# Kernel tuning notes

Measured on AMD Instinct MI355X. Metric: run time of the kernel, lower is better.

The kernel has to match this reference:

```python
import jax, jax.numpy as jnp
import numpy as np

N, E = 50000, 800000
IN, HID, HEADS, OUT = 128, 32, 8, 40
D1 = HID * HEADS  # 256


def setup_inputs() -> dict:
    key = jax.random.key(0)
    ks = jax.random.split(key, 24)

    def w(k, fin, fout):
        return (jax.random.normal(k, (fin, fout), jnp.float32) / np.sqrt(fin)).astype(jnp.float32)

    def b(k, fout):
        return (jax.random.normal(k, (fout,), jnp.float32) * 0.02).astype(jnp.float32)

    inp = {
        "x": jax.random.normal(ks[0], (N, IN), jnp.float32),
        "edge_index": jax.random.randint(ks[1], (2, E), 0, N, dtype=jnp.int64),
        # layer 1: TransformerConv(IN -> HID, heads=HEADS, concat=True, beta=True)
        "q1w": w(ks[2], IN, D1), "q1b": b(ks[3], D1),
        "k1w": w(ks[4], IN, D1), "k1b": b(ks[5], D1),
        "v1w": w(ks[6], IN, D1), "v1b": b(ks[7], D1),
        "s1w": w(ks[8], IN, D1), "s1b": b(ks[9], D1),
        "b1w": w(ks[10], 3 * D1, 1),
        # layer 2: TransformerConv(D1 -> OUT, heads=1, concat=False, beta=True)
        "q2w": w(ks[11], D1, OUT), "q2b": b(ks[12], OUT),
        "k2w": w(ks[13], D1, OUT), "k2b": b(ks[14], OUT),
        "v2w": w(ks[15], D1, OUT), "v2b": b(ks[16], OUT),
        "s2w": w(ks[17], D1, OUT), "s2b": b(ks[18], OUT),
        "b2w": w(ks[19], 3 * OUT, 1),
    }
    return inp


def _tconv(x, src, dst, qw, qb, kw, kb, vw, vb, sw, sb, bw, heads, ch, concat):
    """PyG TransformerConv (no edge_attr, root_weight=True, beta=True), eval mode."""
    n = x.shape[0]
    q = (x @ qw + qb).reshape(n, heads, ch)
    k = (x @ kw + kb).reshape(n, heads, ch)
    v = (x @ vw + vb).reshape(n, heads, ch)
    # per-edge attention logits: message flows src(j) -> dst(i)
    alpha = jnp.einsum("ehc,ehc->eh", q[dst], k[src]) / np.sqrt(ch)  # [E,H]
    # segment softmax over incoming edges of each dst node
    amax = jax.ops.segment_max(alpha, dst, num_segments=n)  # [N,H]
    a = jnp.exp(alpha - amax[dst])
    asum = jax.ops.segment_sum(a, dst, num_segments=n)  # [N,H]
    attn = a / asum[dst]  # [E,H]
    # scatter-aggregate weighted values
    out = jax.ops.segment_sum(v[src] * attn[:, :, None], dst, num_segments=n)  # [N,H,C]
    out = out.reshape(n, heads * ch) if concat else out.mean(axis=1)
    skip = x @ sw + sb
    beta = jax.nn.sigmoid(jnp.concatenate([out, skip, out - skip], axis=-1) @ bw)  # [N,1]
    return beta * skip + (1.0 - beta) * out


def reference(x, edge_index, q1w, q1b, k1w, k1b, v1w, v1b, s1w, s1b, b1w,
              q2w, q2b, k2w, k2b, v2w, v2b, s2w, s2b, b2w):
    src, dst = edge_index[0], edge_index[1]
    h = jax.nn.elu(_tconv(x, src, dst, q1w, q1b, k1w, k1b, v1w, v1b, s1w, s1b, b1w, HEADS, HID, True))
    return _tconv(h, src, dst, q2w, q2b, k2w, k2b, v2w, v2b, s2w, s2b, b2w, 1, OUT, False)
```

## Files before the change

### kernel.cpp

```cpp
#include <hip/hip_runtime.h>
#include <cstdint>
#include <cstddef>

#define N_NODES 50000
#define N_EDGES 800000
#define IN_F    128
#define HID     32
#define HEADS   8
#define OUT_F   40
#define D1      256
#define W1COLS  1024
#define W2COLS  160
#define CAP     64

#define GFILL_B   3125
#define G1_BX     391
#define G1_BY     8
#define G1_GEMM_B (G1_BX * G1_BY)
#define G1_TOTAL  (GFILL_B + G1_GEMM_B)

typedef unsigned short ushortT;
typedef unsigned char  ucharT;
typedef unsigned long long ullT;
typedef unsigned short ushortx8 __attribute__((ext_vector_type(8)));
typedef __bf16 bf16x8 __attribute__((ext_vector_type(8)));
typedef float floatx4 __attribute__((ext_vector_type(4)));
typedef float floatx2 __attribute__((ext_vector_type(2)));

__device__ inline ushortT f2bf(float f) {
    union { float f; unsigned int u; } c; c.f = f;
    unsigned int r = c.u + 0x7FFFu + ((c.u >> 16) & 1u);
    return (ushortT)(r >> 16);
}
__device__ inline float bf2f(ushortT h) {
    union { unsigned int u; float f; } c; c.u = ((unsigned int)h) << 16; return c.f;
}

__device__ inline float red8(float x) {
    int v;
    v = __builtin_amdgcn_update_dpp(0, __float_as_int(x), 0xB1, 0xF, 0xF, false);
    x += __int_as_float(v);
    v = __builtin_amdgcn_update_dpp(0, __float_as_int(x), 0x4E, 0xF, 0xF, false);
    x += __int_as_float(v);
    v = __builtin_amdgcn_update_dpp(0, __float_as_int(x), 0x141, 0xF, 0xF, false);
    x += __int_as_float(v);
    return x;
}

#define PREP_CONV_B  6250
#define PREP_W1_B    512
#define PREP_W2_B    160
#define PREP_TOTAL_B (PREP_CONV_B + PREP_W1_B + PREP_W2_B)

__global__ __launch_bounds__(256) void k_prep(
        const float* __restrict__ x, ushortT* __restrict__ xb,
        const float* __restrict__ q1w, const float* __restrict__ k1w,
        const float* __restrict__ v1w, const float* __restrict__ s1w,
        const float* __restrict__ q1b, const float* __restrict__ k1b,
        const float* __restrict__ v1b, const float* __restrict__ s1b,
        ushortT* __restrict__ W1T, float* __restrict__ b1c,
        const float* __restrict__ q2w, const float* __restrict__ k2w,
        const float* __restrict__ v2w, const float* __restrict__ s2w,
        const float* __restrict__ q2b, const float* __restrict__ k2b,
        const float* __restrict__ v2b, const float* __restrict__ s2b,
        ushortT* __restrict__ W2T, float* __restrict__ b2c) {
    int b = blockIdx.x;
    int tid = threadIdx.x;
    if (b < PREP_CONV_B) {
        int i = b * 256 + tid;
        float4 v = reinterpret_cast<const float4*>(x)[i];
        ushort4 o;
        o.x = f2bf(v.x); o.y = f2bf(v.y); o.z = f2bf(v.z); o.w = f2bf(v.w);
        reinterpret_cast<ushort4*>(xb)[i] = o;
    } else if (b < PREP_CONV_B + PREP_W1_B) {
        int t = (b - PREP_CONV_B) * 256 + tid;
        int c = t / IN_F, k = t % IN_F;
        int sel = c >> 8, cc = c & 255;
        const float* w = sel == 0 ? q1w : sel == 1 ? k1w : sel == 2 ? v1w : s1w;
        W1T[(size_t)c * IN_F + k] = f2bf(w[(size_t)k * D1 + cc]);
        if (k == 0) {
            const float* bb = sel == 0 ? q1b : sel == 1 ? k1b : sel == 2 ? v1b : s1b;
            b1c[c] = bb[cc];
        }
    } else {
        int t = (b - PREP_CONV_B - PREP_W1_B) * 256 + tid;
        int c = t / D1, k = t % D1;
        int sel = c / OUT_F, cc = c % OUT_F;
        const float* w = sel == 0 ? q2w : sel == 1 ? k2w : sel == 2 ? v2w : s2w;
        W2T[(size_t)c * D1 + k] = f2bf(w[(size_t)k * OUT_F + cc]);
        if (k == 0) {
            const float* bb = sel == 0 ? q2b : sel == 1 ? k2b : sel == 2 ? v2b : s2b;
            b2c[c] = bb[cc];
        }
    }
}

template<int MODE>
__global__ __launch_bounds__(256) void gemm_mfma_pack(
        const ushortT* __restrict__ A, const ushortT* __restrict__ BT,
        const float* __restrict__ bias, float* __restrict__ QSf,
        ushortT* __restrict__ QSh, ucharT* __restrict__ KV8,
        ushortT* __restrict__ K2V2,
        const int* __restrict__ ei, int* __restrict__ cursor, int* __restrict__ col,
        int M, int K, int Nn) {
    constexpr int TM = 128, TN = 128, TK = 32, LDP = 40;
    __shared__ ushortT smem[TM * LDP + TN * LDP];
    ushortT* As = smem;
    ushortT* Bs = smem + TM * LDP;
    int bx2, by2;
    if (MODE == 1) {
        int t = blockIdx.x;
        int idx;
        bool isFill;
        if (t < 2 * GFILL_B) { isFill = !(t & 1); idx = t >> 1; }
        else                 { isFill = false;    idx = t - GFILL_B; }
        if (isFill) {
            int e = idx * 256 + threadIdx.x;
            if (e < N_EDGES) {
                int dd = ei[N_EDGES + e];
                int p = atomicAdd(&cursor[dd], 1);
                col[dd * CAP + p] = ei[e];
            }
            return;
        }
        bx2 = idx % G1_BX;
        by2 = idx / G1_BX;
    } else {
        bx2 = blockIdx.x;
        by2 = blockIdx.y;
    }
    int tid = threadIdx.x;
    int lane = tid & 63, wave = tid >> 6;
    int bm = bx2 * TM, bn = by2 * TN;
    int wm = (wave & 1) * 64, wn = (wave >> 1) * 64;
    int mrow = lane & 15, g = lane >> 4;
    floatx4 acc[4][4] = {};

    for (int k0 = 0; k0 < K; k0 += TK) {
#pragma unroll
        for (int it = 0; it < 2; ++it) {
            int idx = tid + it * 256;
            int r = idx >> 2, c = (idx & 3) * 8;
            int gm = bm + r;
            ushortx8 val;
            if (gm < M) val = *reinterpret_cast<const ushortx8*>(A + (size_t)gm * K + k0 + c);
            else        val = (ushortx8)0;
            *reinterpret_cast<ushortx8*>(As + r * LDP + c) = val;
        }
#pragma unroll
        for (int it = 0; it < 2; ++it) {
            int idx = tid + it * 256;
            int r = idx >> 2, c = (idx & 3) * 8;
            int gn = bn + r;
            ushortx8 val;
            if (gn < Nn) val = *reinterpret_cast<const ushortx8*>(BT + (size_t)gn * K + k0 + c);
            else         val = (ushortx8)0;
            *reinterpret_cast<ushortx8*>(Bs + r * LDP + c) = val;
        }
        __syncthreads();
        {
            bf16x8 a[4], b[4];
#pragma unroll
            for (int i = 0; i < 4; ++i)
                a[i] = *reinterpret_cast<const bf16x8*>(As + (wm + i * 16 + mrow) * LDP + g * 8);
#pragma unroll
            for (int j = 0; j < 4; ++j)
                b[j] = *reinterpret_cast<const bf16x8*>(Bs + (wn + j * 16 + mrow) * LDP + g * 8);
#pragma unroll
            for (int i = 0; i < 4; ++i)
#pragma unroll
                for (int j = 0; j < 4; ++j)
                    acc[i][j] = __builtin_amdgcn_mfma_f32_16x16x32_bf16(a[i], b[j], acc[i][j], 0, 0, 0);
        }
        __syncthreads();
    }

    if (MODE == 1) {
        float* lds = reinterpret_cast<float*>(smem) + wave * 1088;
        int sec = by2 >> 1;
        int ccbase = (by2 & 1) * 128 + wn;
        int cb4 = (lane & 15) * 4;
        int rlo = lane >> 4;
        float4 bv = *reinterpret_cast<const float4*>(bias + by2 * 128 + wn + cb4);
#pragma unroll
        for (int i = 0; i < 4; ++i) {
#pragma unroll
            for (int j = 0; j < 4; ++j)
#pragma unroll
                for (int r = 0; r < 4; ++r)
                    lds[(g * 4 + r) * 68 + j * 16 + mrow] = acc[i][j][r];
#pragma unroll
            for (int it = 0; it < 4; ++it) {
                int row = it * 4 + rlo;
                int gm = bm + wm + i * 16 + row;
                if (gm >= M) continue;
                float4 v = *reinterpret_cast<float4*>(lds + row * 68 + cb4);
                v.x += bv.x; v.y += bv.y; v.z += bv.z; v.w += bv.w;
                int cc = ccbase + cb4;
                if (sec == 0 || sec == 3) {
                    ushort4 h;
                    h.x = f2bf(v.x); h.y = f2bf(v.y); h.z = f2bf(v.z); h.w = f2bf(v.w);
                    ushortT* dst = QSh + (size_t)gm * 512 + (sec == 3 ? 256 : 0) + cc;
                    *reinterpret_cast<ushort4*>(dst) = h;
                } else {
                    unsigned int pk = 0;
                    pk = __builtin_amdgcn_cvt_pk_fp8_f32(v.x, v.y, pk, false);
                    pk = __builtin_amdgcn_cvt_pk_fp8_f32(v.z, v.w, pk, true);
                    ucharT* dst = KV8 + (size_t)gm * 512 + cc * 2 + (sec == 2 ? 4 : 0);
                    *reinterpret_cast<unsigned int*>(dst) = pk;
                }
            }
        }
    } else {
#pragma unroll
        for (int i = 0; i < 4; ++i) {
#pragma unroll
            for (int j = 0; j < 4; ++j) {
                int gn = bn + wn + j * 16 + mrow;
                if (gn >= Nn) continue;
                float bvs = bias[gn];
#pragma unroll
                for (int r = 0; r < 4; ++r) {
                    int gm = bm + wm + i * 16 + g * 4 + r;
                    if (gm >= M) continue;
                    float val = acc[i][j][r] + bvs;
                    int sec = gn / OUT_F, cc = gn % OUT_F;
                    if (sec == 0)      QSf[(size_t)gm * 80 + cc] = val;
                    else if (sec == 1) K2V2[(size_t)gm * 80 + cc] = f2bf(val);
                    else if (sec == 2) K2V2[(size_t)gm * 80 + 40 + cc] = f2bf(val);
                    else               QSf[(size_t)gm * 80 + 40 + cc] = val;
                }
            }
        }
    }
}

__global__ __launch_bounds__(256) void k_edge1(
        const ushortT* __restrict__ QSh, const ucharT* __restrict__ KV8,
        const float* __restrict__ bw,
        const int* __restrict__ degc, const int* __restrict__ col,
        ushortT* __restrict__ H1b) {
    int gid  = blockIdx.x * blockDim.x + threadIdx.x;
    int lane = threadIdx.x & 63;
    int node = __builtin_amdgcn_readfirstlane(gid >> 6);
    if (node >= N_NODES) return;
    const float scale = 0.17677669529663687f;
    ushort4 qh = *reinterpret_cast<const ushort4*>(QSh + (size_t)node * 512 + lane * 4);
    floatx2 q01, q23;
    q01[0] = bf2f(qh.x) * scale; q01[1] = bf2f(qh.y) * scale;
    q23[0] = bf2f(qh.z) * scale; q23[1] = bf2f(qh.w) * scale;

    float l = 0.f;
    floatx2 acc01 = {0.f, 0.f}, acc23 = {0.f, 0.f};
    const int* colp = col + node * CAP;
    int d = degc[node];
    int voff = lane * 8;
    int t = 0;
    for (; t + 4 <= d; t += 4) {
        int4 js = *reinterpret_cast<const int4*>(colp + t);
        const ucharT* r0 = KV8 + ((size_t)js.x << 9);
        const ucharT* r1 = KV8 + ((size_t)js.y << 9);
        const ucharT* r2 = KV8 + ((size_t)js.z << 9);
        const ucharT* r3 = KV8 + ((size_t)js.w << 9);
        ullT kv0 = *reinterpret_cast<const ullT*>(r0 + voff);
        ullT kv1 = *reinterpret_cast<const ullT*>(r1 + voff);
        ullT kv2 = *reinterpret_cast<const ullT*>(r2 + voff);
        ullT kv3 = *reinterpret_cast<const ullT*>(r3 + voff);
        floatx2 k0a = __builtin_amdgcn_cvt_pk_f32_fp8((unsigned)kv0, false);
        floatx2 k0b = __builtin_amdgcn_cvt_pk_f32_fp8((unsigned)kv0, true);
        floatx2 k1a = __builtin_amdgcn_cvt_pk_f32_fp8((unsigned)kv1, false);
        floatx2 k1b = __builtin_amdgcn_cvt_pk_f32_fp8((unsigned)kv1, true);
        floatx2 k2a = __builtin_amdgcn_cvt_pk_f32_fp8((unsigned)kv2, false);
        floatx2 k2b = __builtin_amdgcn_cvt_pk_f32_fp8((unsigned)kv2, true);
        floatx2 k3a = __builtin_amdgcn_cvt_pk_f32_fp8((unsigned)kv3, false);
        floatx2 k3b = __builtin_amdgcn_cvt_pk_f32_fp8((unsigned)kv3, true);
        floatx2 pd0 = q01 * k0a + q23 * k0b;
        floatx2 pd1 = q01 * k1a + q23 * k1b;
        floatx2 pd2 = q01 * k2a + q23 * k2b;
        floatx2 pd3 = q01 * k3a + q23 * k3b;
        float p0 = red8(pd0[0] + pd0[1]);
        float p1 = red8(pd1[0] + pd1[1]);
        float p2 = red8(pd2[0] + pd2[1]);
        float p3 = red8(pd3[0] + pd3[1]);
        float e0 = __expf(p0);
        float e1 = __expf(p1);
        float e2 = __expf(p2);
        float e3 = __expf(p3);
        l += (e0 + e1) + (e2 + e3);
        floatx2 v0a = __builtin_amdgcn_cvt_pk_f32_fp8((unsigned)(kv0 >> 32), false);
        floatx2 v0b = __builtin_amdgcn_cvt_pk_f32_fp8((unsigned)(kv0 >> 32), true);
        floatx2 v1a = __builtin_amdgcn_cvt_pk_f32_fp8((unsigned)(kv1 >> 32), false);
        floatx2 v1b = __builtin_amdgcn_cvt_pk_f32_fp8((unsigned)(kv1 >> 32), true);
        floatx2 v2a = __builtin_amdgcn_cvt_pk_f32_fp8((unsigned)(kv2 >> 32), false);
        floatx2 v2b = __builtin_amdgcn_cvt_pk_f32_fp8((unsigned)(kv2 >> 32), true);
        floatx2 v3a = __builtin_amdgcn_cvt_pk_f32_fp8((unsigned)(kv3 >> 32), false);
        floatx2 v3b = __builtin_amdgcn_cvt_pk_f32_fp8((unsigned)(kv3 >> 32), true);
        floatx2 e0v = {e0, e0}, e1v = {e1, e1}, e2v = {e2, e2}, e3v = {e3, e3};
        acc01 += e0v * v0a; acc23 += e0v * v0b;
        acc01 += e1v * v1a; acc23 += e1v * v1b;
        acc01 += e2v * v2a; acc23 += e2v * v2b;
        acc01 += e3v * v3a; acc23 += e3v * v3b;
    }
    for (; t < d; ++t) {
        int j = colp[t];
        ullT kv = *reinterpret_cast<const ullT*>(KV8 + ((size_t)j << 9) + voff);
        floatx2 ka = __builtin_amdgcn_cvt_pk_f32_fp8((unsigned)kv, false);
        floatx2 kb = __builtin_amdgcn_cvt_pk_f32_fp8((unsigned)kv, true);
        floatx2 pd = q01 * ka + q23 * kb;
        float p = red8(pd[0] + pd[1]);
        float e = __expf(p);
        l += e;
        floatx2 va = __builtin_amdgcn_cvt_pk_f32_fp8((unsigned)(kv >> 32), false);
        floatx2 vb = __builtin_amdgcn_cvt_pk_f32_fp8((unsigned)(kv >> 32), true);
        floatx2 ev = {e, e};
        acc01 += ev * va; acc23 += ev * vb;
    }
    float inv = (l > 0.f) ? 1.f / l : 0.f;
    float4 o = make_float4(acc01[0] * inv, acc01[1] * inv, acc23[0] * inv, acc23[1] * inv);
    ushort4 sh = *reinterpret_cast<const ushort4*>(QSh + (size_t)node * 512 + 256 + lane * 4);
    float4 sk;
    sk.x = bf2f(sh.x); sk.y = bf2f(sh.y); sk.z = bf2f(sh.z); sk.w = bf2f(sh.w);
    const int c4 = lane * 4;
    float4 w0 = *reinterpret_cast<const float4*>(bw + c4);
    float4 w1 = *reinterpret_cast<const float4*>(bw + D1 + c4);
    float4 w2 = *reinterpret_cast<const float4*>(bw + 2 * D1 + c4);
    float part = o.x * w0.x + o.y * w0.y + o.z * w0.z + o.w * w0.w
               + sk.x * w1.x + sk.y * w1.y + sk.z * w1.z + sk.w * w1.w
               + (o.x - sk.x) * w2.x + (o.y - sk.y) * w2.y
               + (o.z - sk.z) * w2.z + (o.w - sk.w) * w2.w;
#pragma unroll
    for (int s = 1; s < 64; s <<= 1) part += __shfl_xor(part, s);
    float beta = 1.f / (1.f + __expf(-part));
    float4 h;
    h.x = beta * sk.x + (1.f - beta) * o.x;
    h.y = beta * sk.y + (1.f - beta) * o.y;
    h.z = beta * sk.z + (1.f - beta) * o.z;
    h.w = beta * sk.w + (1.f - beta) * o.w;
    h.x = h.x > 0.f ? h.x : __expf(h.x) - 1.f;
    h.y = h.y > 0.f ? h.y : __expf(h.y) - 1.f;
    h.z = h.z > 0.f ? h.z : __expf(h.z) - 1.f;
    h.w = h.w > 0.f ? h.w : __expf(h.w) - 1.f;
    ushort4 hb;
    hb.x = f2bf(h.x); hb.y = f2bf(h.y); hb.z = f2bf(h.z); hb.w = f2bf(h.w);
    *reinterpret_cast<ushort4*>(H1b + (size_t)node * D1 + c4) = hb;
}

__global__ __launch_bounds__(256) void k_edge2(
        const float* __restrict__ QS, const ushortT* __restrict__ K2V2,
        const float* __restrict__ bw,
        const int* __restrict__ degc, const int* __restrict__ col,
        float* __restrict__ out) {
    __shared__ float        qbuf[4][40];
    __shared__ float        attn[4][64];
    __shared__ int          jb[4][64];
    __shared__ unsigned int ksm[4][64 * 21];
    int gid  = blockIdx.x * blockDim.x + threadIdx.x;
    int node = gid >> 6;
    int wave = threadIdx.x >> 6;
    int lane = threadIdx.x & 63;
    if (node >= N_NODES) return;
    const float scale = 0.15811388300841897f;
    bool act = lane < OUT_F;
    if (act) qbuf[wave][lane] = QS[(size_t)node * 80 + lane] * scale;

    int d = degc[node];
    if (lane < d) jb[wave][lane] = col[node * CAP + lane];

    const unsigned int* Kdw = reinterpret_cast<const unsigned int*>(K2V2);
    int sr = lane / 20;
    int sc = lane - sr * 20;
    for (int r0 = 0; r0 < d; r0 += 3) {
        int rr = r0 + sr;
        if (lane < 60 && rr < d)
            ksm[wave][rr * 21 + sc] = Kdw[(size_t)jb[wave][rr] * 40 + sc];
    }

    float p = 0.f;
    if (lane < d) {
        float s = 0.f;
#pragma unroll
        for (int c = 0; c < 20; ++c) {
            unsigned int kk = ksm[wave][lane * 21 + c];
            s += qbuf[wave][2 * c]     * bf2f((ushortT)(kk & 0xFFFFu))
               + qbuf[wave][2 * c + 1] * bf2f((ushortT)(kk >> 16));
        }
        p = __expf(s);
    }
    attn[wave][lane] = p;
    float l = p;
#pragma unroll
    for (int s = 1; s < 64; s <<= 1) l += __shfl_xor(l, s);

    float acc = 0.f;
    int ln = act ? lane : 0;
    int e = 0;
    for (; e + 4 <= d; e += 4) {
        int je0 = jb[wave][e],     je1 = jb[wave][e + 1];
        int je2 = jb[wave][e + 2], je3 = jb[wave][e + 3];
        float v0 = bf2f(K2V2[(size_t)je0 * 80 + 40 + ln]);
        float v1 = bf2f(K2V2[(size_t)je1 * 80 + 40 + ln]);
        float v2 = bf2f(K2V2[(size_t)je2 * 80 + 40 + ln]);
        float v3 = bf2f(K2V2[(size_t)je3 * 80 + 40 + ln]);
        acc += (attn[wave][e] * v0 + attn[wave][e + 1] * v1)
             + (attn[wave][e + 2] * v2 + attn[wave][e + 3] * v3);
    }
    for (; e < d; ++e)
        acc += attn[wave][e] * bf2f(K2V2[(size_t)jb[wave][e] * 80 + 40 + ln]);

    float inv = (l > 0.f) ? 1.f / l : 0.f;
    float o  = acc * inv;
    float sk = act ? QS[(size_t)node * 80 + 40 + lane] : 0.f;
    float part = act ? (o * bw[lane] + sk * bw[OUT_F + lane] + (o - sk) * bw[2 * OUT_F + lane]) : 0.f;
#pragma unroll
    for (int s = 1; s < 64; s <<= 1) part += __shfl_xor(part, s);
    float beta = 1.f / (1.f + __expf(-part));
    if (act) out[(size_t)node * OUT_F + lane] = beta * sk + (1.f - beta) * o;
}

extern "C" void kernel_launch(void* const* d_in, const int* in_sizes, int n_in,
                              void* d_out, int out_size, void* d_ws, size_t ws_size,
                              hipStream_t stream) {
    const float* x   = (const float*)d_in[0];
    const int*   ei  = (const int*)d_in[1];
    const float* q1w = (const float*)d_in[2];
    const float* q1b = (const float*)d_in[3];
    const float* k1w = (const float*)d_in[4];
    const float* k1b = (const float*)d_in[5];
    const float* v1w = (const float*)d_in[6];
    const float* v1b = (const float*)d_in[7];
    const float* s1w = (const float*)d_in[8];
    const float* s1b = (const float*)d_in[9];
    const float* b1w = (const float*)d_in[10];
    const float* q2w = (const float*)d_in[11];
    const float* q2b = (const float*)d_in[12];
    const float* k2w = (const float*)d_in[13];
    const float* k2b = (const float*)d_in[14];
    const float* v2w = (const float*)d_in[15];
    const float* v2b = (const float*)d_in[16];
    const float* s2w = (const float*)d_in[17];
    const float* s2b = (const float*)d_in[18];
    const float* b2w = (const float*)d_in[19];
    float* out = (float*)d_out;

    char* w = (char*)d_ws;
    ushortT* QSh = (ushortT*)w;
    ucharT*  KV8 = (ucharT*)(w + 51200000);
    ushortT* H1b = (ushortT*)(w + 102400000);
    ushortT* xb  = (ushortT*)(w + 128000000);
    ushortT* W1T = (ushortT*)(w + 140800000);
    ushortT* W2T = (ushortT*)(w + 141062144);
    float*   b1c = (float*)(w + 141144064);
    float*   b2c = (float*)(w + 141148160);
    int* cursor  = (int*)(w + 141149184);
    int* col     = cursor + N_NODES;
    float*   QS2  = (float*)w;
    ushortT* K2V2 = (ushortT*)(w + 51200000);

    hipMemsetAsync(cursor, 0, N_NODES * sizeof(int), stream);

    k_prep<<<PREP_TOTAL_B, 256, 0, stream>>>(
        x, xb,
        q1w, k1w, v1w, s1w, q1b, k1b, v1b, s1b, W1T, b1c,
        q2w, k2w, v2w, s2w, q2b, k2b, v2b, s2b, W2T, b2c);

    gemm_mfma_pack<1><<<G1_TOTAL, 256, 0, stream>>>(
        xb, W1T, b1c, nullptr, QSh, KV8, nullptr,
        ei, cursor, col, N_NODES, IN_F, W1COLS);

    k_edge1<<<(N_NODES * 64) / 256, 256, 0, stream>>>(QSh, KV8, b1w, cursor, col, H1b);

    dim3 g2((N_NODES + 127) / 128, (W2COLS + 127) / 128);
    gemm_mfma_pack<2><<<g2, 256, 0, stream>>>(H1b, W2T, b2c, QS2, nullptr, nullptr,
                                              K2V2, nullptr, nullptr, nullptr,
                                              N_NODES, D1, W2COLS);

    k_edge2<<<(N_NODES * 64) / 256, 256, 0, stream>>>(QS2, K2V2, b2w, cursor, col, out);
}
```

Before: 350.5 us.

## Split KV8 rows into K and V halves, assign lanes to K or V

The layer-1 GEMM epilogue now writes all K values into the first 256 bytes of each node row and all V values into the last 256, instead of interleaving them. In k_edge1, lanes 0-31 each take 8 K channels to compute the attention logit, reduced over 4 lanes with two DPP steps. A shuffle then broadcasts the exp weight to lanes 32-63, which accumulate 8 V channels each and handle the skip, beta gate and ELU output. This cuts the cross-lane reduction per edge but adds a shuffle per edge, and half of the accumulate and finalize work is now redundant or idle.

```diff
diff --git a/kernel.cpp b/kernel.cpp
--- a/kernel.cpp
+++ b/kernel.cpp
@@ -34,17 +34,6 @@
 }
 __device__ inline float bf2f(ushortT h) {
     union { unsigned int u; float f; } c; c.u = ((unsigned int)h) << 16; return c.f;
-}
-
-__device__ inline float red8(float x) {
-    int v;
-    v = __builtin_amdgcn_update_dpp(0, __float_as_int(x), 0xB1, 0xF, 0xF, false);
-    x += __int_as_float(v);
-    v = __builtin_amdgcn_update_dpp(0, __float_as_int(x), 0x4E, 0xF, 0xF, false);
-    x += __int_as_float(v);
-    v = __builtin_amdgcn_update_dpp(0, __float_as_int(x), 0x141, 0xF, 0xF, false);
-    x += __int_as_float(v);
-    return x;
 }
 
 #define PREP_CONV_B  6250
@@ -206,7 +195,7 @@
                     unsigned int pk = 0;
                     pk = __builtin_amdgcn_cvt_pk_fp8_f32(v.x, v.y, pk, false);
                     pk = __builtin_amdgcn_cvt_pk_fp8_f32(v.z, v.w, pk, true);
-                    ucharT* dst = KV8 + (size_t)gm * 512 + cc * 2 + (sec == 2 ? 4 : 0);
+                    ucharT* dst = KV8 + (size_t)gm * 512 + (sec == 2 ? 256 : 0) + cc;
                     *reinterpret_cast<unsigned int*>(dst) = pk;
                 }
             }
@@ -245,104 +234,100 @@
     int node = __builtin_amdgcn_readfirstlane(gid >> 6);
     if (node >= N_NODES) return;
     const float scale = 0.17677669529663687f;
-    ushort4 qh = *reinterpret_cast<const ushort4*>(QSh + (size_t)node * 512 + lane * 4);
-    floatx2 q01, q23;
-    q01[0] = bf2f(qh.x) * scale; q01[1] = bf2f(qh.y) * scale;
-    q23[0] = bf2f(qh.z) * scale; q23[1] = bf2f(qh.w) * scale;
+    bool isV = lane >= 32;
+    ushortx8 qs8 = *reinterpret_cast<const ushortx8*>(QSh + (size_t)node * 512 + lane * 8);
+    float qsc = isV ? 1.0f : scale;
+    floatx2 q01, q23, q45, q67;
+    q01[0] = bf2f(qs8[0]) * qsc; q01[1] = bf2f(qs8[1]) * qsc;
+    q23[0] = bf2f(qs8[2]) * qsc; q23[1] = bf2f(qs8[3]) * qsc;
+    q45[0] = bf2f(qs8[4]) * qsc; q45[1] = bf2f(qs8[5]) * qsc;
+    q67[0] = bf2f(qs8[6]) * qsc; q67[1] = bf2f(qs8[7]) * qsc;
 
     float l = 0.f;
-    floatx2 acc01 = {0.f, 0.f}, acc23 = {0.f, 0.f};
+    floatx2 acc0 = {0.f, 0.f}, acc1 = {0.f, 0.f}, acc2 = {0.f, 0.f}, acc3 = {0.f, 0.f};
     const int* colp = col + node * CAP;
     int d = degc[node];
     int voff = lane * 8;
+
+#define EDGE_BODY(kv) do {                                                              \
+    floatx2 a0 = __builtin_amdgcn_cvt_pk_f32_fp8((unsigned)(kv), false);                \
+    floatx2 a1 = __builtin_amdgcn_cvt_pk_f32_fp8((unsigned)(kv), true);                 \
+    floatx2 a2 = __builtin_amdgcn_cvt_pk_f32_fp8((unsigned)((kv) >> 32), false);        \
+    floatx2 a3 = __builtin_amdgcn_cvt_pk_f32_fp8((unsigned)((kv) >> 32), true);         \
+    floatx2 pd = q01 * a0 + q23 * a1 + q45 * a2 + q67 * a3;                             \
+    float p = pd[0] + pd[1];                                                            \
+    p += __int_as_float(__builtin_amdgcn_update_dpp(                                    \
+             0, __float_as_int(p), 0xB1, 0xF, 0xF, false));    \
+    p += __int_as_float(__builtin_amdgcn_update_dpp(                                    \
+             0, __float_as_int(p), 0x4E, 0xF, 0xF, false));    \
+    float e = __expf(p);                                                                \
+    float eb = __shfl(e, lane & 31);             \
+    l += eb;                                                                            \
+    floatx2 ev = {eb, eb};                                                              \
+    acc0 += ev * a0; acc1 += ev * a1; acc2 += ev * a2; acc3 += ev * a3;                 \
+} while (0)
+
     int t = 0;
     for (; t + 4 <= d; t += 4) {
         int4 js = *reinterpret_cast<const int4*>(colp + t);
-        const ucharT* r0 = KV8 + ((size_t)js.x << 9);
-        const ucharT* r1 = KV8 + ((size_t)js.y << 9);
-        const ucharT* r2 = KV8 + ((size_t)js.z << 9);
-        const ucharT* r3 = KV8 + ((size_t)js.w << 9);
-        ullT kv0 = *reinterpret_cast<const ullT*>(r0 + voff);
-        ullT kv1 = *reinterpret_cast<const ullT*>(r1 + voff);
-        ullT kv2 = *reinterpret_cast<const ullT*>(r2 + voff);
-        ullT kv3 = *reinterpret_cast<const ullT*>(r3 + voff);
-        floatx2 k0a = __builtin_amdgcn_cvt_pk_f32_fp8((unsigned)kv0, false);
-        floatx2 k0b = __builtin_amdgcn_cvt_pk_f32_fp8((unsigned)kv0, true);
-        floatx2 k1a = __builtin_amdgcn_cvt_pk_f32_fp8((unsigned)kv1, false);
-        floatx2 k1b = __builtin_amdgcn_cvt_pk_f32_fp8((unsigned)kv1, true);
-        floatx2 k2a = __builtin_amdgcn_cvt_pk_f32_fp8((unsigned)kv2, false);
-        floatx2 k2b = __builtin_amdgcn_cvt_pk_f32_fp8((unsigned)kv2, true);
-        floatx2 k3a = __builtin_amdgcn_cvt_pk_f32_fp8((unsigned)kv3, false);
-        floatx2 k3b = __builtin_amdgcn_cvt_pk_f32_fp8((unsigned)kv3, true);
-        floatx2 pd0 = q01 * k0a + q23 * k0b;
-        floatx2 pd1 = q01 * k1a + q23 * k1b;
-        floatx2 pd2 = q01 * k2a + q23 * k2b;
-        floatx2 pd3 = q01 * k3a + q23 * k3b;
-        float p0 = red8(pd0[0] + pd0[1]);
-        float p1 = red8(pd1[0] + pd1[1]);
-        float p2 = red8(pd2[0] + pd2[1]);
-        float p3 = red8(pd3[0] + pd3[1]);
-        float e0 = __expf(p0);
-        float e1 = __expf(p1);
-        float e2 = __expf(p2);
-        float e3 = __expf(p3);
-        l += (e0 + e1) + (e2 + e3);
-        floatx2 v0a = __builtin_amdgcn_cvt_pk_f32_fp8((unsigned)(kv0 >> 32), false);
-        floatx2 v0b = __builtin_amdgcn_cvt_pk_f32_fp8((unsigned)(kv0 >> 32), true);
-        floatx2 v1a = __builtin_amdgcn_cvt_pk_f32_fp8((unsigned)(kv1 >> 32), false);
-        floatx2 v1b = __builtin_amdgcn_cvt_pk_f32_fp8((unsigned)(kv1 >> 32), true);
-        floatx2 v2a = __builtin_amdgcn_cvt_pk_f32_fp8((unsigned)(kv2 >> 32), false);
-        floatx2 v2b = __builtin_amdgcn_cvt_pk_f32_fp8((unsigned)(kv2 >> 32), true);
-        floatx2 v3a = __builtin_amdgcn_cvt_pk_f32_fp8((unsigned)(kv3 >> 32), false);
-        floatx2 v3b = __builtin_amdgcn_cvt_pk_f32_fp8((unsigned)(kv3 >> 32), true);
-        floatx2 e0v = {e0, e0}, e1v = {e1, e1}, e2v = {e2, e2}, e3v = {e3, e3};
-        acc01 += e0v * v0a; acc23 += e0v * v0b;
-        acc01 += e1v * v1a; acc23 += e1v * v1b;
-        acc01 += e2v * v2a; acc23 += e2v * v2b;
-        acc01 += e3v * v3a; acc23 += e3v * v3b;
+        ullT kv0 = *reinterpret_cast<const ullT*>(KV8 + ((size_t)js.x << 9) + voff);
+        ullT kv1 = *reinterpret_cast<const ullT*>(KV8 + ((size_t)js.y << 9) + voff);
+        ullT kv2 = *reinterpret_cast<const ullT*>(KV8 + ((size_t)js.z << 9) + voff);
+        ullT kv3 = *reinterpret_cast<const ullT*>(KV8 + ((size_t)js.w << 9) + voff);
+        EDGE_BODY(kv0);
+        EDGE_BODY(kv1);
+        EDGE_BODY(kv2);
+        EDGE_BODY(kv3);
     }
     for (; t < d; ++t) {
         int j = colp[t];
         ullT kv = *reinterpret_cast<const ullT*>(KV8 + ((size_t)j << 9) + voff);
-        floatx2 ka = __builtin_amdgcn_cvt_pk_f32_fp8((unsigned)kv, false);
-        floatx2 kb = __builtin_amdgcn_cvt_pk_f32_fp8((unsigned)kv, true);
-        floatx2 pd = q01 * ka + q23 * kb;
-        float p = red8(pd[0] + pd[1]);
-        float e = __expf(p);
-        l += e;
-        floatx2 va = __builtin_amdgcn_cvt_pk_f32_fp8((unsigned)(kv >> 32), false);
-        floatx2 vb = __builtin_amdgcn_cvt_pk_f32_fp8((unsigned)(kv >> 32), true);
-        floatx2 ev = {e, e};
-        acc01 += ev * va; acc23 += ev * vb;
-    }
+        EDGE_BODY(kv);
+    }
+#undef EDGE_BODY
+
     float inv = (l > 0.f) ? 1.f / l : 0.f;
-    float4 o = make_float4(acc01[0] * inv, acc01[1] * inv, acc23[0] * inv, acc23[1] * inv);
-    ushort4 sh = *reinterpret_cast<const ushort4*>(QSh + (size_t)node * 512 + 256 + lane * 4);
-    float4 sk;
-    sk.x = bf2f(sh.x); sk.y = bf2f(sh.y); sk.z = bf2f(sh.z); sk.w = bf2f(sh.w);
-    const int c4 = lane * 4;
-    float4 w0 = *reinterpret_cast<const float4*>(bw + c4);
-    float4 w1 = *reinterpret_cast<const float4*>(bw + D1 + c4);
-    float4 w2 = *reinterpret_cast<const float4*>(bw + 2 * D1 + c4);
-    float part = o.x * w0.x + o.y * w0.y + o.z * w0.z + o.w * w0.w
-               + sk.x * w1.x + sk.y * w1.y + sk.z * w1.z + sk.w * w1.w
-               + (o.x - sk.x) * w2.x + (o.y - sk.y) * w2.y
-               + (o.z - sk.z) * w2.z + (o.w - sk.w) * w2.w;
-#pragma unroll
-    for (int s = 1; s < 64; s <<= 1) part += __shfl_xor(part, s);
+    floatx2 iv = {inv, inv};
+    floatx2 o0 = acc0 * iv, o1 = acc1 * iv, o2 = acc2 * iv, o3 = acc3 * iv;
+    int cb = isV ? (lane - 32) * 8 : 0;
+    float4 wa0 = *reinterpret_cast<const float4*>(bw + cb);
+    float4 wa1 = *reinterpret_cast<const float4*>(bw + cb + 4);
+    float4 wb0 = *reinterpret_cast<const float4*>(bw + D1 + cb);
+    float4 wb1 = *reinterpret_cast<const float4*>(bw + D1 + cb + 4);
+    float4 wc0 = *reinterpret_cast<const float4*>(bw + 2 * D1 + cb);
+    float4 wc1 = *reinterpret_cast<const float4*>(bw + 2 * D1 + cb + 4);
+    float part = 0.f;
+    if (isV) {
+        part = o0[0] * wa0.x + o0[1] * wa0.y + o1[0] * wa0.z + o1[1] * wa0.w
+             + o2[0] * wa1.x + o2[1] * wa1.y + o3[0] * wa1.z + o3[1] * wa1.w
+             + q01[0] * wb0.x + q01[1] * wb0.y + q23[0] * wb0.z + q23[1] * wb0.w
+             + q45[0] * wb1.x + q45[1] * wb1.y + q67[0] * wb1.z + q67[1] * wb1.w
+             + (o0[0] - q01[0]) * wc0.x + (o0[1] - q01[1]) * wc0.y
+             + (o1[0] - q23[0]) * wc0.z + (o1[1] - q23[1]) * wc0.w
+             + (o2[0] - q45[0]) * wc1.x + (o2[1] - q45[1]) * wc1.y
+             + (o3[0] - q67[0]) * wc1.z + (o3[1] - q67[1]) * wc1.w;
+    }
+#pragma unroll
+    for (int s = 1; s < 32; s <<= 1) part += __shfl_xor(part, s);
     float beta = 1.f / (1.f + __expf(-part));
-    float4 h;
-    h.x = beta * sk.x + (1.f - beta) * o.x;
-    h.y = beta * sk.y + (1.f - beta) * o.y;
-    h.z = beta * sk.z + (1.f - beta) * o.z;
-    h.w = beta * sk.w + (1.f - beta) * o.w;
-    h.x = h.x > 0.f ? h.x : __expf(h.x) - 1.f;
-    h.y = h.y > 0.f ? h.y : __expf(h.y) - 1.f;
-    h.z = h.z > 0.f ? h.z : __expf(h.z) - 1.f;
-    h.w = h.w > 0.f ? h.w : __expf(h.w) - 1.f;
-    ushort4 hb;
-    hb.x = f2bf(h.x); hb.y = f2bf(h.y); hb.z = f2bf(h.z); hb.w = f2bf(h.w);
-    *reinterpret_cast<ushort4*>(H1b + (size_t)node * D1 + c4) = hb;
+    if (isV) {
+        float h[8];
+        h[0] = beta * q01[0] + (1.f - beta) * o0[0];
+        h[1] = beta * q01[1] + (1.f - beta) * o0[1];
+        h[2] = beta * q23[0] + (1.f - beta) * o1[0];
+        h[3] = beta * q23[1] + (1.f - beta) * o1[1];
+        h[4] = beta * q45[0] + (1.f - beta) * o2[0];
+        h[5] = beta * q45[1] + (1.f - beta) * o2[1];
+        h[6] = beta * q67[0] + (1.f - beta) * o3[0];
+        h[7] = beta * q67[1] + (1.f - beta) * o3[1];
+        ushortx8 hb;
+#pragma unroll
+        for (int c = 0; c < 8; ++c) {
+            float hv = h[c] > 0.f ? h[c] : __expf(h[c]) - 1.f;
+            hb[c] = f2bf(hv);
+        }
+        *reinterpret_cast<ushortx8*>(H1b + (size_t)node * D1 + (lane - 32) * 8) = hb;
+    }
 }
 
 __global__ __launch_bounds__(256) void k_edge2(
```

After: 349.6 us. No clear change (-0.3%).
